# Performance work log

Hardware: AMD Instinct MI355X
Metric: run time of the kernel (lower is better)

## Reference

```python
import jax, jax.numpy as jnp
import numpy as np


def setup_inputs() -> dict:
    key = jax.random.key(0)
    ks = jax.random.split(key, 20)
    B, T, D, H, FC, O = 256, 256, 256, 512, 256, 2
    s = 0.02
    inp = {
        "x": jax.random.normal(ks[0], (B, T, D), jnp.float32),
        "time": jax.random.uniform(ks[1], (B, T, 1), jnp.float32),
        "Wi_w": jax.random.normal(ks[2], (H, D), jnp.float32) * s,
        "Wi_b": jnp.zeros((H,), jnp.float32),
        "Ui_w": jax.random.normal(ks[3], (H, H), jnp.float32) * s,
        "Ui_b": jnp.zeros((H,), jnp.float32),
        "bi": jnp.zeros((H,), jnp.float32),
        "Wf_w": jax.random.normal(ks[4], (H, D), jnp.float32) * s,
        "Wf_b": jnp.zeros((H,), jnp.float32),
        "Uf_w": jax.random.normal(ks[5], (H, H), jnp.float32) * s,
        "Uf_b": jnp.zeros((H,), jnp.float32),
        "bf": jnp.ones((H,), jnp.float32),
        "Wo_w": jax.random.normal(ks[6], (H, D), jnp.float32) * s,
        "Wo_b": jnp.zeros((H,), jnp.float32),
        "Uo_w": jax.random.normal(ks[7], (H, H), jnp.float32) * s,
        "Uo_b": jnp.zeros((H,), jnp.float32),
        "bo": jnp.zeros((H,), jnp.float32),
        "Wc_w": jax.random.normal(ks[8], (H, D), jnp.float32) * s,
        "Wc_b": jnp.zeros((H,), jnp.float32),
        "Uc_w": jax.random.normal(ks[9], (H, H), jnp.float32) * s,
        "Uc_b": jnp.zeros((H,), jnp.float32),
        "bc": jnp.zeros((H,), jnp.float32),
        "Wd_w": jax.random.normal(ks[10], (H, H), jnp.float32) * s,
        "b_decomp": jnp.ones((H,), jnp.float32),
        "fc_w": jax.random.normal(ks[11], (FC, H), jnp.float32) * s,
        "fc_b": jnp.zeros((FC,), jnp.float32),
        "cls_w": jax.random.normal(ks[12], (O, FC), jnp.float32) * s,
        "cls_b": jnp.zeros((O,), jnp.float32),
    }
    return inp


def reference(x, time, Wi_w, Wi_b, Ui_w, Ui_b, bi, Wf_w, Wf_b, Uf_w, Uf_b, bf,
              Wo_w, Wo_b, Uo_w, Uo_b, bo, Wc_w, Wc_b, Uc_w, Uc_b, bc,
              Wd_w, b_decomp, fc_w, fc_b, cls_w, cls_b):
    B, T, D = x.shape
    H = Ui_w.shape[0]
    # Precompute input-side gate projections across all timesteps (batched GEMM),
    # folding both the Linear bias and the extra per-gate parameter.
    xi = jnp.einsum('btd,hd->bth', x, Wi_w) + (Wi_b + bi)
    xf = jnp.einsum('btd,hd->bth', x, Wf_w) + (Wf_b + bf)
    xo = jnp.einsum('btd,hd->bth', x, Wo_w) + (Wo_b + bo)
    xc = jnp.einsum('btd,hd->bth', x, Wc_w) + (Wc_b + bc)
    # map_elapse_time: 1 / log(t + 2.7183), shape [B, T]
    Tmap = 1.0 / jnp.log(time[:, :, 0] + 2.7183)

    def step(carry, inp):
        h, c = carry
        xi_t, xf_t, xo_t, xc_t, Tt = inp  # [B,H] x4, [B]
        # time-decayed cell decomposition
        c_st = jnp.tanh(c @ Wd_w.T + b_decomp)
        c = c - c_st + Tt[:, None] * c_st
        i_t = jax.nn.sigmoid(xi_t + h @ Ui_w.T + Ui_b)
        f_t = jax.nn.sigmoid(xf_t + h @ Uf_w.T + Uf_b)
        o_t = jax.nn.sigmoid(xo_t + h @ Uo_w.T + Uo_b)
        c_hat = jnp.tanh(xc_t + h @ Uc_w.T + Uc_b)
        c = f_t * c + i_t * c_hat
        h = o_t * jnp.tanh(c)
        return (h, c), None

    h0 = jnp.zeros((B, H), x.dtype)
    c0 = jnp.zeros((B, H), x.dtype)
    scan_in = (jnp.swapaxes(xi, 0, 1), jnp.swapaxes(xf, 0, 1),
               jnp.swapaxes(xo, 0, 1), jnp.swapaxes(xc, 0, 1),
               jnp.swapaxes(Tmap, 0, 1))
    (h_T, _), _ = jax.lax.scan(step, (h0, c0), scan_in)
    # Only the last step's classifier output is returned by the original module.
    # Dropout is identity in eval mode.
    fc_out = jax.nn.relu(h_T @ fc_w.T + fc_b)
    return fc_out @ cls_w.T + cls_b
```

## Files before the change

kernel.cpp:

```cpp
#include <hip/hip_runtime.h>


#define T_STEPS 256
#define BATCH   256
#define DIN     256
#define HID     512

typedef __attribute__((ext_vector_type(8))) __bf16 bf16x8;
typedef __attribute__((ext_vector_type(4))) float  f32x4;

#define MFMA(a,b,c) __builtin_amdgcn_mfma_f32_16x16x32_bf16((a),(b),(c),0,0,0)

#define H_S     0
#define C_S     16640
#define X_S     33280
#define WIN_S   41728
#define Z_S     109312
#define LDS_SZ  128896
#define HSTR    1040
#define XSTR    528
#define ZROW    17

struct ScanP {
  const float *x, *tim;
  const float *Wi_w,*Wi_b,*Ui_w,*Ui_b,*bi;
  const float *Wf_w,*Wf_b,*Uf_w,*Uf_b,*bf_;
  const float *Wo_w,*Wo_b,*Uo_w,*Uo_b,*bo;
  const float *Wc_w,*Wc_b,*Uc_w,*Uc_b,*bc;
  const float *Wd_w,*b_dec;
  unsigned long long *hc_buf;
  float *h_final;
  unsigned int *flags;
};

__device__ __forceinline__ float fsigm(float z){ return 1.f/(1.f + __expf(-z)); }
__device__ __forceinline__ float ftanh(float z){
  float e = __expf(-2.f*fabsf(z));
  float t = (1.f - e)/(1.f + e);
  return z < 0.f ? -t : t;
}

__device__ __forceinline__ uint4 cld16(const void* p){
  uint4 r;
  asm volatile("global_load_dwordx4 %0, %1, off sc0 sc1"
               : "=v"(r) : "v"(p) : "memory");
  return r;
}
__device__ __forceinline__ void cst8(void* p, unsigned long long v){
  asm volatile("global_store_dwordx2 %0, %1, off sc0 sc1"
               :: "v"(p), "v"(v) : "memory");
}

__device__ __forceinline__ bf16x8 wfrag8(const float* p){
  const float4* p4 = (const float4*)p;
  float4 a = p4[0], b = p4[1];
  bf16x8 r = { (__bf16)a.x,(__bf16)a.y,(__bf16)a.z,(__bf16)a.w,
               (__bf16)b.x,(__bf16)b.y,(__bf16)b.z,(__bf16)b.w };
  return r;
}
__device__ __forceinline__ void zstore(char* L, int tile, int lane, f32x4 v){
  float* p = (float*)(L + Z_S) + tile*(16*ZROW) + ((lane>>4)*4)*ZROW + (lane&15);
  p[0]=v[0]; p[ZROW]=v[1]; p[2*ZROW]=v[2]; p[3*ZROW]=v[3];
}
__device__ __forceinline__ float zread(const char* L, int tile, int r, int c){
  return ((const float*)(L + Z_S))[tile*(16*ZROW) + r*ZROW + c];
}

__global__ void __launch_bounds__(256, 1) tlstm_scan(ScanP P)
{
  __shared__ __align__(16) char L[LDS_SZ];
  const int tid  = threadIdx.x;
  const int bid  = blockIdx.x;
  const int g    = bid & 15;
  const int cs   = bid >> 4;
  const int rbase = g * 16;
  const int cbase = cs * 32;
  const int wave = tid >> 6, lane = tid & 63, lo = lane & 15, hi = lane >> 4;
  const int nt   = wave & 1;
  const int gp   = wave >> 1;
  const int g0   = gp * 2, g1 = g0 + 1;

  {
    const float* Wg = (wave == 0) ? P.Wi_w : (wave == 1) ? P.Wf_w
                    : (wave == 2) ? P.Wo_w : P.Wc_w;
    const int wc = lane >> 1, q2 = lane & 1;
    const float4* src = (const float4*)(Wg + (size_t)(cbase + wc) * DIN + q2 * 128);
    char* dst = L + WIN_S + (size_t)(wave * 32 + wc) * XSTR + q2 * 256;
#pragma unroll
    for (int j = 0; j < 16; j++){
      float4 a = src[2*j], b = src[2*j+1];
      bf16x8 o = { (__bf16)a.x,(__bf16)a.y,(__bf16)a.z,(__bf16)a.w,
                   (__bf16)b.x,(__bf16)b.y,(__bf16)b.z,(__bf16)b.w };
      *(bf16x8*)(dst + j*16) = o;
    }
  }

  bf16x8 bP[16], bQ[16], bR[16];
  {
    const float* Pw = (gp == 0) ? P.Ui_w : P.Uo_w;
    const float* Qw = (gp == 0) ? P.Uf_w : P.Uc_w;
    const size_t colb = (size_t)(cbase + nt * 16 + lo) * HID;
#pragma unroll
    for (int kc = 0; kc < 16; kc++){
      bP[kc] = wfrag8(Pw + colb + kc * 32 + hi * 8);
      bQ[kc] = wfrag8(Qw + colb + kc * 32 + hi * 8);
    }
    if (wave >= 2){
#pragma unroll
      for (int kc = 0; kc < 16; kc++)
        bR[kc] = wfrag8(P.Wd_w + colb + kc * 32 + hi * 8);
    }
  }

  const int erow = tid >> 4;
  const int ecp  = (tid & 15) * 2;
  float bias_i[2], bias_f[2], bias_o[2], bias_c[2], bias_d[2], cr[2];
#pragma unroll
  for (int e = 0; e < 2; e++){
    int c = cbase + ecp + e;
    bias_i[e] = P.Wi_b[c] + P.bi[c]  + P.Ui_b[c];
    bias_f[e] = P.Wf_b[c] + P.bf_[c] + P.Uf_b[c];
    bias_o[e] = P.Wo_b[c] + P.bo[c]  + P.Uo_b[c];
    bias_c[e] = P.Wc_b[c] + P.bc[c]  + P.Uc_b[c];
    bias_d[e] = P.b_dec[c];
    cr[e] = 0.f;
  }

  const int srow = tid >> 4, sseg = tid & 15;
  const size_t pub_off = ((size_t)(rbase + erow) * 256 + cs * 16 + (tid & 15)) * 8;

  __syncthreads();

  float4 xv[4];
  float tvr;
  {
    const float4* xs = (const float4*)(P.x + ((size_t)(rbase + srow) * T_STEPS) * DIN + sseg * 16);
#pragma unroll
    for (int j = 0; j < 4; j++) xv[j] = xs[j];
    tvr = P.tim[(size_t)(rbase + erow) * T_STEPS];
  }

#pragma unroll 1
  for (int t = 0; t < T_STEPS; ++t){
    const int rp = t & 1;
    const char* hcprev = (const char*)(P.hc_buf + (size_t)rp * BATCH * 256);
    char* hcnext = (char*)(P.hc_buf + (size_t)(rp ^ 1) * BATCH * 256);

    const float tv = tvr;
    {
      char* dst = L + X_S + srow * XSTR + sseg * 32;
#pragma unroll
      for (int j = 0; j < 2; j++){
        float4 a = xv[2*j], b = xv[2*j+1];
        bf16x8 o = { (__bf16)a.x,(__bf16)a.y,(__bf16)a.z,(__bf16)a.w,
                     (__bf16)b.x,(__bf16)b.y,(__bf16)b.z,(__bf16)b.w };
        *(bf16x8*)(dst + j*16) = o;
      }
    }
    __syncthreads();

    f32x4 xA = {0.f,0.f,0.f,0.f}, xB = xA;
#pragma unroll
    for (int q = 0; q < 8; q++){
      bf16x8 ax = *(const bf16x8*)(L + X_S + lo * XSTR + q*64 + hi*16);
      bf16x8 w0 = *(const bf16x8*)(L + WIN_S + (size_t)(g0*32 + nt*16 + lo) * XSTR + q*64 + hi*16);
      bf16x8 w1 = *(const bf16x8*)(L + WIN_S + (size_t)(g1*32 + nt*16 + lo) * XSTR + q*64 + hi*16);
      xA = MFMA(ax, w0, xA);
      xB = MFMA(ax, w1, xB);
    }
    zstore(L, 10+g0*2+nt, lane, xA);
    zstore(L, 10+g1*2+nt, lane, xB);

    uint4 gr[8];
    const char* src = hcprev + (size_t)(rbase + wave * 4) * 2048;
#pragma unroll
    for (int j = 0; j < 8; j++){
      int row = j >> 1;
      int gg  = (j & 1) * 64 + lane;
      gr[j] = cld16(src + (size_t)row * 2048 + (size_t)gg * 16);
    }
    asm volatile("s_waitcnt vmcnt(0)" ::: "memory");
    __builtin_amdgcn_sched_barrier(0);

    {
      const unsigned int expv = (unsigned int)(t & 1)
                              | ((unsigned int)((t >> 1) & 1) << 16);
      unsigned int stale = 0;
#pragma unroll
      for (int j = 0; j < 8; j++){
        unsigned int bad = ((gr[j].x ^ expv) | (gr[j].y ^ expv)
                          | (gr[j].z ^ expv) | (gr[j].w ^ expv)) & 0x00010001u;
        stale |= (bad ? 1u : 0u) << j;
      }
      int guard = 0;
      while (__any((int)stale) && ++guard < 65536){
#pragma unroll
        for (int j = 0; j < 8; j++){
          if (stale & (1u << j)){
            int row = j >> 1;
            int gg  = (j & 1) * 64 + lane;
            gr[j] = cld16(src + (size_t)row * 2048 + (size_t)gg * 16);
          }
        }
        asm volatile("s_waitcnt vmcnt(0)" ::: "memory");
        __builtin_amdgcn_sched_barrier(0);
        unsigned int ns = 0;
#pragma unroll
        for (int j = 0; j < 8; j++){
          if (stale & (1u << j)){
            unsigned int bad = ((gr[j].x ^ expv) | (gr[j].y ^ expv)
                              | (gr[j].z ^ expv) | (gr[j].w ^ expv)) & 0x00010001u;
            ns |= (bad ? 1u : 0u) << j;
          }
        }
        stale = ns;
      }
    }

    if (t < T_STEPS - 1){
      const float4* xs = (const float4*)(P.x + ((size_t)(rbase + srow) * T_STEPS + (t + 1)) * DIN + sseg * 16);
#pragma unroll
      for (int j = 0; j < 4; j++) xv[j] = xs[j];
      tvr = P.tim[(size_t)(rbase + erow) * T_STEPS + (t + 1)];
    }

    {
#pragma unroll
      for (int j = 0; j < 8; j++){
        int row = wave * 4 + (j >> 1);
        int gg  = (j & 1) * 64 + lane;
        *(uint2*)(L + H_S + row * HSTR + gg * 8) = uint2{gr[j].x, gr[j].z};
        *(uint2*)(L + C_S + row * HSTR + gg * 8) = uint2{gr[j].y, gr[j].w};
      }
    }
    __syncthreads();

    {
      f32x4 zA = {0.f,0.f,0.f,0.f}, zB = zA, zD = zA;
#pragma unroll
      for (int kc = 0; kc < 16; kc++){
        bf16x8 a = *(const bf16x8*)(L + H_S + lo * HSTR + kc*64 + hi*16);
        zA = MFMA(a, bP[kc], zA);
        zB = MFMA(a, bQ[kc], zB);
      }
      if (wave >= 2){
#pragma unroll
        for (int kc = 0; kc < 16; kc++){
          bf16x8 a = *(const bf16x8*)(L + C_S + lo * HSTR + kc*64 + hi*16);
          zD = MFMA(a, bR[kc], zD);
        }
      }
      zstore(L, g0*2+nt, lane, zA);
      zstore(L, g1*2+nt, lane, zB);
      if (wave >= 2) zstore(L, 8+nt, lane, zD);
    }
    __syncthreads();

    {
      float Tmap = 1.f / __logf(tv + 2.7183f);
      unsigned int hpk = 0, cpk = 0;
      float hv2[2];
#pragma unroll
      for (int e = 0; e < 2; e++){
        int col = ecp + e;
        int ntc = col >> 4, cl = col & 15;
        float zi = zread(L, 0+ntc,  erow, cl) + zread(L, 10+0+ntc,  erow, cl) + bias_i[e];
        float zf = zread(L, 2+ntc,  erow, cl) + zread(L, 10+2+ntc,  erow, cl) + bias_f[e];
        float zo = zread(L, 4+ntc,  erow, cl) + zread(L, 10+4+ntc,  erow, cl) + bias_o[e];
        float zc = zread(L, 6+ntc,  erow, cl) + zread(L, 10+6+ntc,  erow, cl) + bias_c[e];
        float zdv = zread(L, 8+ntc, erow, cl) + bias_d[e];
        float cst = ftanh(zdv);
        float c1  = cr[e] - cst + Tmap * cst;
        float ig = fsigm(zi), fg = fsigm(zf), og = fsigm(zo);
        float ch = ftanh(zc);
        float c2 = fg * c1 + ig * ch;
        float hv_ = og * ftanh(c2);
        cr[e] = c2; hv2[e] = hv_;
        hpk |= (unsigned int)__builtin_bit_cast(unsigned short, (__bf16)hv_) << (16*e);
        cpk |= (unsigned int)__builtin_bit_cast(unsigned short, (__bf16)c2) << (16*e);
      }
      if (t < T_STEPS - 1){
        const unsigned int wtag  = (unsigned int)((t + 1) & 3);
        const unsigned int tmask = (wtag & 1u) | ((wtag >> 1) << 16);
        hpk = (hpk & 0xFFFEFFFEu) | tmask;
        cpk = (cpk & 0xFFFEFFFEu) | tmask;
        cst8(hcnext + pub_off,
             (unsigned long long)hpk | ((unsigned long long)cpk << 32));
      } else {
        size_t off = (size_t)(rbase + erow) * HID + cbase + ecp;
        P.h_final[off]     = hv2[0];
        P.h_final[off + 1] = hv2[1];
      }
    }
  }
}

__global__ void __launch_bounds__(256) tlstm_head(const float* __restrict__ hfin,
    const float* __restrict__ fc_w, const float* __restrict__ fc_b,
    const float* __restrict__ cls_w, const float* __restrict__ cls_b,
    float* __restrict__ out)
{
  __shared__ float hrow[512];
  __shared__ float fcv[256];
  const int b = blockIdx.x, tid = threadIdx.x;
  ((float2*)hrow)[tid] = ((const float2*)(hfin + (size_t)b * 512))[tid];
  __syncthreads();
  {
    const float4* w4 = (const float4*)(fc_w + (size_t)tid * 512);
    const float4* h4 = (const float4*)hrow;
    float acc = fc_b[tid];
#pragma unroll 4
    for (int k = 0; k < 128; k++){
      float4 w = w4[k], h = h4[k];
      acc += w.x*h.x + w.y*h.y + w.z*h.z + w.w*h.w;
    }
    fcv[tid] = fmaxf(acc, 0.f);
  }
  __syncthreads();
  const int wave = tid >> 6, lane = tid & 63;
  if (wave < 2){
    const float* cw = cls_w + wave * 256;
    float s = 0.f;
#pragma unroll
    for (int j = lane; j < 256; j += 64) s += fcv[j] * cw[j];
#pragma unroll
    for (int off = 32; off > 0; off >>= 1) s += __shfl_down(s, off, 64);
    if (lane == 0) out[b * 2 + wave] = s + cls_b[wave];
  }
}

extern "C" void kernel_launch(void* const* d_in, const int* in_sizes, int n_in,
                              void* d_out, int out_size, void* d_ws, size_t ws_size,
                              hipStream_t stream)
{
  (void)in_sizes; (void)n_in; (void)out_size; (void)ws_size;

  ScanP P;
  P.x    = (const float*)d_in[0];
  P.tim  = (const float*)d_in[1];
  P.Wi_w = (const float*)d_in[2];  P.Wi_b = (const float*)d_in[3];
  P.Ui_w = (const float*)d_in[4];  P.Ui_b = (const float*)d_in[5];  P.bi  = (const float*)d_in[6];
  P.Wf_w = (const float*)d_in[7];  P.Wf_b = (const float*)d_in[8];
  P.Uf_w = (const float*)d_in[9];  P.Uf_b = (const float*)d_in[10]; P.bf_ = (const float*)d_in[11];
  P.Wo_w = (const float*)d_in[12]; P.Wo_b = (const float*)d_in[13];
  P.Uo_w = (const float*)d_in[14]; P.Uo_b = (const float*)d_in[15]; P.bo  = (const float*)d_in[16];
  P.Wc_w = (const float*)d_in[17]; P.Wc_b = (const float*)d_in[18];
  P.Uc_w = (const float*)d_in[19]; P.Uc_b = (const float*)d_in[20]; P.bc  = (const float*)d_in[21];
  P.Wd_w = (const float*)d_in[22]; P.b_dec = (const float*)d_in[23];
  const float* fc_w  = (const float*)d_in[24];
  const float* fc_b  = (const float*)d_in[25];
  const float* cls_w = (const float*)d_in[26];
  const float* cls_b = (const float*)d_in[27];

  unsigned long long* hc_buf = (unsigned long long*)d_ws;
  unsigned int* flags = (unsigned int*)(hc_buf + 2 * BATCH * 256);
  float* h_final = (float*)((char*)flags + 1024);
  P.hc_buf = hc_buf; P.h_final = h_final; P.flags = flags;

  const size_t zero_bytes = (size_t)2 * BATCH * 256 * 8 + 1024;
  hipMemsetAsync(d_ws, 0, zero_bytes, stream);

  hipLaunchKernelGGL(tlstm_scan, dim3(256), dim3(256), 0, stream, P);
  hipLaunchKernelGGL(tlstm_head, dim3(256), dim3(256), 0, stream,
                     h_final, fc_w, fc_b, cls_w, cls_b, (float*)d_out);
}
```

Measured before the change: 904.9 us.

## Double-buffer input projection tiles to drop per-step barrier before input MFMA

Moves the bf16 conversion and LDS store of the next step's x tile to just before the existing barrier after the recurrent MFMAs. This removes the barrier at the top of each timestep. The input projection results move to a new parity-indexed LDS region, so the next step's writes cannot clobber values still being read. The x global load is issued earlier in the step, and the time load is no longer prefetched. LDS use grows by about 8.7 KB.

```diff
diff --git a/kernel.cpp b/kernel.cpp
--- a/kernel.cpp
+++ b/kernel.cpp
@@ -16,7 +16,8 @@
 #define X_S     33280
 #define WIN_S   41728
 #define Z_S     109312
-#define LDS_SZ  128896
+#define Z2_S    120192
+#define LDS_SZ  137600
 #define HSTR    1040
 #define XSTR    528
 #define ZROW    17
@@ -64,6 +65,13 @@
 }
 __device__ __forceinline__ float zread(const char* L, int tile, int r, int c){
   return ((const float*)(L + Z_S))[tile*(16*ZROW) + r*ZROW + c];
+}
+__device__ __forceinline__ void z2store(char* L, int par, int tile, int lane, f32x4 v){
+  float* p = (float*)(L + Z2_S) + (par*8 + tile)*(16*ZROW) + ((lane>>4)*4)*ZROW + (lane&15);
+  p[0]=v[0]; p[ZROW]=v[1]; p[2*ZROW]=v[2]; p[3*ZROW]=v[3];
+}
+__device__ __forceinline__ float z2read(const char* L, int par, int tile, int r, int c){
+  return ((const float*)(L + Z2_S))[(par*8 + tile)*(16*ZROW) + r*ZROW + c];
 }
 
 __global__ void __launch_bounds__(256, 1) tlstm_scan(ScanP P)
@@ -129,35 +137,35 @@
   const int srow = tid >> 4, sseg = tid & 15;
   const size_t pub_off = ((size_t)(rbase + erow) * 256 + cs * 16 + (tid & 15)) * 8;
 
-  __syncthreads();
-
   float4 xv[4];
-  float tvr;
   {
     const float4* xs = (const float4*)(P.x + ((size_t)(rbase + srow) * T_STEPS) * DIN + sseg * 16);
 #pragma unroll
     for (int j = 0; j < 4; j++) xv[j] = xs[j];
-    tvr = P.tim[(size_t)(rbase + erow) * T_STEPS];
-  }
+    char* dst = L + X_S + srow * XSTR + sseg * 32;
+#pragma unroll
+    for (int j = 0; j < 2; j++){
+      float4 a = xv[2*j], b = xv[2*j+1];
+      bf16x8 o = { (__bf16)a.x,(__bf16)a.y,(__bf16)a.z,(__bf16)a.w,
+                   (__bf16)b.x,(__bf16)b.y,(__bf16)b.z,(__bf16)b.w };
+      *(bf16x8*)(dst + j*16) = o;
+    }
+  }
+  __syncthreads();
 
 #pragma unroll 1
   for (int t = 0; t < T_STEPS; ++t){
     const int rp = t & 1;
+    const int p2 = t & 1;
     const char* hcprev = (const char*)(P.hc_buf + (size_t)rp * BATCH * 256);
     char* hcnext = (char*)(P.hc_buf + (size_t)(rp ^ 1) * BATCH * 256);
 
-    const float tv = tvr;
-    {
-      char* dst = L + X_S + srow * XSTR + sseg * 32;
-#pragma unroll
-      for (int j = 0; j < 2; j++){
-        float4 a = xv[2*j], b = xv[2*j+1];
-        bf16x8 o = { (__bf16)a.x,(__bf16)a.y,(__bf16)a.z,(__bf16)a.w,
-                     (__bf16)b.x,(__bf16)b.y,(__bf16)b.z,(__bf16)b.w };
-        *(bf16x8*)(dst + j*16) = o;
-      }
-    }
-    __syncthreads();
+    if (t < T_STEPS - 1){
+      const float4* xs = (const float4*)(P.x + ((size_t)(rbase + srow) * T_STEPS + (t + 1)) * DIN + sseg * 16);
+#pragma unroll
+      for (int j = 0; j < 4; j++) xv[j] = xs[j];
+    }
+    const float tv = P.tim[(size_t)(rbase + erow) * T_STEPS + t];
 
     f32x4 xA = {0.f,0.f,0.f,0.f}, xB = xA;
 #pragma unroll
@@ -168,8 +176,8 @@
       xA = MFMA(ax, w0, xA);
       xB = MFMA(ax, w1, xB);
     }
-    zstore(L, 10+g0*2+nt, lane, xA);
-    zstore(L, 10+g1*2+nt, lane, xB);
+    z2store(L, p2, g0*2+nt, lane, xA);
+    z2store(L, p2, g1*2+nt, lane, xB);
 
     uint4 gr[8];
     const char* src = hcprev + (size_t)(rbase + wave * 4) * 2048;
@@ -217,13 +225,6 @@
       }
     }
 
-    if (t < T_STEPS - 1){
-      const float4* xs = (const float4*)(P.x + ((size_t)(rbase + srow) * T_STEPS + (t + 1)) * DIN + sseg * 16);
-#pragma unroll
-      for (int j = 0; j < 4; j++) xv[j] = xs[j];
-      tvr = P.tim[(size_t)(rbase + erow) * T_STEPS + (t + 1)];
-    }
-
     {
 #pragma unroll
       for (int j = 0; j < 8; j++){
@@ -254,6 +255,16 @@
       zstore(L, g1*2+nt, lane, zB);
       if (wave >= 2) zstore(L, 8+nt, lane, zD);
     }
+    if (t < T_STEPS - 1){
+      char* dst = L + X_S + srow * XSTR + sseg * 32;
+#pragma unroll
+      for (int j = 0; j < 2; j++){
+        float4 a = xv[2*j], b = xv[2*j+1];
+        bf16x8 o = { (__bf16)a.x,(__bf16)a.y,(__bf16)a.z,(__bf16)a.w,
+                     (__bf16)b.x,(__bf16)b.y,(__bf16)b.z,(__bf16)b.w };
+        *(bf16x8*)(dst + j*16) = o;
+      }
+    }
     __syncthreads();
 
     {
@@ -264,10 +275,10 @@
       for (int e = 0; e < 2; e++){
         int col = ecp + e;
         int ntc = col >> 4, cl = col & 15;
-        float zi = zread(L, 0+ntc,  erow, cl) + zread(L, 10+0+ntc,  erow, cl) + bias_i[e];
-        float zf = zread(L, 2+ntc,  erow, cl) + zread(L, 10+2+ntc,  erow, cl) + bias_f[e];
-        float zo = zread(L, 4+ntc,  erow, cl) + zread(L, 10+4+ntc,  erow, cl) + bias_o[e];
-        float zc = zread(L, 6+ntc,  erow, cl) + zread(L, 10+6+ntc,  erow, cl) + bias_c[e];
+        float zi = zread(L, 0+ntc,  erow, cl) + z2read(L, p2, 0+ntc, erow, cl) + bias_i[e];
+        float zf = zread(L, 2+ntc,  erow, cl) + z2read(L, p2, 2+ntc, erow, cl) + bias_f[e];
+        float zo = zread(L, 4+ntc,  erow, cl) + z2read(L, p2, 4+ntc, erow, cl) + bias_o[e];
+        float zc = zread(L, 6+ntc,  erow, cl) + z2read(L, p2, 6+ntc, erow, cl) + bias_c[e];
         float zdv = zread(L, 8+ntc, erow, cl) + bias_d[e];
         float cst = ftanh(zdv);
         float c1  = cr[e] - cst + Tmap * cst;
```

New measurement: 869.3 us (median of 2 runs). 3.9% less time.
